# Performance work log

Hardware: AMD Instinct MI355X
Metric: run time of the kernel (lower is better)

## Reference

```python
import jax, jax.numpy as jnp
import numpy as np

B, N, H, E, P = 2, 20000, 128, 200000, 3


def _mlp2(x, w1, b1, w2, b2):
    # Linear -> SiLU -> Linear
    return jax.nn.silu(x @ w1 + b1) @ w2 + b2


def setup_inputs() -> dict:
    key = jax.random.key(0)
    ks = iter(jax.random.split(key, 40))
    def nrm(shape, s=0.05):
        return jax.random.normal(next(ks), shape, dtype=jnp.float32) * s
    inp = {
        "features": jax.random.normal(next(ks), (B, N, H), dtype=jnp.float32),
        "positions": jax.random.normal(next(ks), (B, N, P), dtype=jnp.float32),
        "edge_index_up": jax.random.randint(next(ks), (2, E), 0, N, dtype=jnp.int32),
        "edge_index_down": jax.random.randint(next(ks), (2, E), 0, N, dtype=jnp.int32),
        "degree_up": jax.random.uniform(next(ks), (N,), minval=1.0, maxval=32.0, dtype=jnp.float32),
        "degree_down": jax.random.uniform(next(ks), (N,), minval=1.0, maxval=32.0, dtype=jnp.float32),
    }
    for name in ("up", "down"):
        inp[f"w_msg1_{name}"] = nrm((2 * H + 1, H)); inp[f"b_msg1_{name}"] = jnp.zeros((H,), jnp.float32)
        inp[f"w_msg2_{name}"] = nrm((H, H));         inp[f"b_msg2_{name}"] = jnp.zeros((H,), jnp.float32)
        inp[f"w_pos1_{name}"] = nrm((H, H));         inp[f"b_pos1_{name}"] = jnp.zeros((H,), jnp.float32)
        inp[f"w_pos2_{name}"] = nrm((H, 1));         inp[f"b_pos2_{name}"] = jnp.zeros((1,), jnp.float32)
    inp["w_upd1"] = nrm((2 * H, H)); inp["b_upd1"] = jnp.zeros((H,), jnp.float32)
    inp["w_upd2"] = nrm((H, H));     inp["b_upd2"] = jnp.zeros((H,), jnp.float32)
    return inp


def reference(features, positions, edge_index_up, edge_index_down, degree_up, degree_down,
              w_msg1_up, b_msg1_up, w_msg2_up, b_msg2_up,
              w_pos1_up, b_pos1_up, w_pos2_up, b_pos2_up,
              w_msg1_down, b_msg1_down, w_msg2_down, b_msg2_down,
              w_pos1_down, b_pos1_down, w_pos2_down, b_pos2_down,
              w_upd1, b_upd1, w_upd2, b_upd2):
    n_neighborhoods = 2
    msg_acc = jnp.zeros_like(features)
    pos_upd = jnp.zeros_like(positions)
    neighborhoods = [
        (edge_index_up, degree_up,
         (w_msg1_up, b_msg1_up, w_msg2_up, b_msg2_up),
         (w_pos1_up, b_pos1_up, w_pos2_up, b_pos2_up)),
        (edge_index_down, degree_down,
         (w_msg1_down, b_msg1_down, w_msg2_down, b_msg2_down),
         (w_pos1_down, b_pos1_down, w_pos2_down, b_pos2_down)),
    ]
    for edge_index, degree, msg_p, pos_p in neighborhoods:
        src, dst = edge_index[0], edge_index[1]
        h_src = features[:, src, :]                     # [B, E, H] gather
        h_dst = features[:, dst, :]                     # [B, E, H] gather
        rel_pos = positions[:, src, :] - positions[:, dst, :]  # [B, E, P]
        dist = jnp.linalg.norm(rel_pos, axis=-1, keepdims=True)  # [B, E, 1]
        msg_input = jnp.concatenate([h_src, h_dst, dist], axis=-1)  # [B, E, 2H+1]
        messages = _mlp2(msg_input, *msg_p)             # [B, E, H]
        agg = jnp.zeros_like(features).at[:, dst, :].add(messages)  # scatter-add over dim 1
        agg = agg / jnp.clip(degree, 1.0, None)[None, :, None]
        msg_acc = msg_acc + agg
        weights = jnp.tanh(_mlp2(messages, *pos_p))     # [B, E, 1]
        pos_upd = pos_upd + jnp.zeros_like(positions).at[:, dst, :].add(weights * rel_pos)
    feat_update = _mlp2(jnp.concatenate([features, msg_acc], axis=-1), w_upd1, b_upd1, w_upd2, b_upd2)
    updated_features = features + feat_update
    updated_positions = positions + pos_upd / n_neighborhoods
    return updated_features, updated_positions
```

## Files before the change

kernel.cpp:

```cpp
#include <hip/hip_runtime.h>

#define BB 2
#define NN 20000
#define HH 128
#define EE 200000
#define EBLK 3125
#define NBLK 79

typedef unsigned short u16;
typedef __attribute__((ext_vector_type(4))) float f32x4;
typedef __bf16 bf16x8 __attribute__((ext_vector_type(8)));

#define MFMA(a, b, c) __builtin_amdgcn_mfma_f32_16x16x32_bf16((a), (b), (c), 0, 0, 0)

__device__ __forceinline__ float bf2f(u16 u) {
    union { unsigned int i; float f; } v; v.i = ((unsigned int)u) << 16; return v.f;
}
__device__ __forceinline__ u16 f2bf(float f) {
    union { __bf16 h; u16 u; } v; v.h = (__bf16)f; return v.u;
}
#if __has_builtin(__builtin_amdgcn_rcpf)
__device__ __forceinline__ float rcpf(float x) { return __builtin_amdgcn_rcpf(x); }
#else
__device__ __forceinline__ float rcpf(float x) { return 1.f / x; }
#endif
__device__ __forceinline__ float silu_f(float z) { return z * rcpf(1.f + __expf(-z)); }
__device__ __forceinline__ float ldv(const void* p, long i, int f) {
    return f ? ((const float*)p)[i] : bf2f(((const u16*)p)[i]);
}

__global__ __launch_bounds__(256) void detect_zero_kernel(const u16* __restrict__ f,
                                                          int* __restrict__ flag,
                                                          int* __restrict__ cnt) {
    int i = blockIdx.x * 256 + threadIdx.x;
    if (i < 40000) cnt[i] = 0;
    if (blockIdx.x == 0) {
        int tid = threadIdx.x;
        u16 v = f[tid * 2];
        int e = (v >> 7) & 0xFF;
        int ok = (e >= 101 && e <= 143) ? 1 : 0;
        __shared__ int c;
        if (tid == 0) c = 0;
        __syncthreads();
        atomicAdd(&c, ok);
        __syncthreads();
        if (tid == 0) *flag = (c < 200) ? 1 : 0;
    }
}

#define C5TOT 5281540
#define FTOT 180224
#define R0 5240000
#define R1 (R0 + C5TOT)
#define R2 (R1 + FTOT)
#define R3 (R2 + 2 * EE)
struct P18 { const void* p[18]; };
struct P8 { const void* w[8]; };

__global__ __launch_bounds__(256) void setup_kernel(
    P18 cp, P8 wf, const int* __restrict__ eu, const int* __restrict__ ed,
    float* __restrict__ ws_acc, u16* __restrict__ canon, u16* __restrict__ fbase,
    int* __restrict__ cnt_up, int* __restrict__ cnt_dn, const int* __restrict__ flag)
{
    long i = (long)blockIdx.x * 256 + threadIdx.x;
    if (i < R0) { ws_acc[i] = 0.f; return; }
    if (i < R1) {
        static const int off[19] = {
            0, 5120000, 5240000, 5260000, 5280000,
            5280128, 5280256, 5280384, 5280512, 5280640,
            5280642, 5280770, 5280898, 5281026, 5281154, 5281282,
            5281284, 5281412, 5281540 };
        static const int rsz[18] = {
            5120000, 120000, 20000, 20000,
            128, 128, 128, 128, 128, 1,
            128, 128, 128, 128, 128, 1,
            128, 128 };
        static const int soff[18] = {
            0, 0, 0, 0,
            32768, 0, 0, 0, 0, 0,
            32768, 0, 0, 0, 0, 0,
            0, 0 };
        int j = (int)(i - R0);
        int isf = *flag;
        int t = 0;
#pragma unroll 1
        while (j >= off[t + 1]) ++t;
        int k = j - off[t];
        u16 v = 0;
        if (k < rsz[t]) v = f2bf(ldv(cp.p[t], (long)soff[t] + k, isf));
        canon[j] = v;
        return;
    }
    if (i < R2) {
        static const int foff[9] = { 0, 32768, 49152, 65536, 98304, 114688,
                                     131072, 163840, 180224 };
        int j = (int)(i - R1);
        int isf = *flag;
        int t = 0;
#pragma unroll 1
        while (j >= foff[t + 1]) ++t;
        int m = j - foff[t];
        int jj = m & 7, lane = (m >> 3) & 63, nt = (m >> 9) & 7, kt = m >> 12;
        int k = kt * 32 + ((lane >> 4) * 8) + jj;
        int n = nt * 16 + (lane & 15);
        fbase[j] = f2bf(ldv(wf.w[t], (long)k * 128 + n, isf));
        return;
    }
    if (i < R3) {
        int e = (int)(i - R2);
        if (e < EE) atomicAdd(&cnt_up[eu[EE + e]], 1);
        else atomicAdd(&cnt_dn[ed[EE + e - EE]], 1);
    }
}

struct SP { const int* cnt[2]; int* cur[2]; int* bsum[2]; };

__global__ __launch_bounds__(256) void scan1_kernel(SP p) {
    int half = blockIdx.x / NBLK;
    int b = blockIdx.x - half * NBLK;
    int t = threadIdx.x;
    int i = b * 256 + t;
    __shared__ int buf[256];
    int v = (i < NN) ? p.cnt[half][i] : 0;
    buf[t] = v;
    __syncthreads();
    for (int s = 1; s < 256; s <<= 1) {
        int x = (t >= s) ? buf[t - s] : 0;
        __syncthreads();
        buf[t] += x;
        __syncthreads();
    }
    if (i < NN) p.cur[half][i] = buf[t] - v;
    if (t == 255) p.bsum[half][b] = buf[255];
}

__global__ __launch_bounds__(256) void scan2_kernel(int* __restrict__ bu, int* __restrict__ bd) {
    __shared__ int buf[2][128];
    int half = threadIdx.x >> 7, t = threadIdx.x & 127;
    int* bs = half ? bd : bu;
    int v = (t < NBLK) ? bs[t] : 0;
    buf[half][t] = v;
    __syncthreads();
    for (int s = 1; s < 128; s <<= 1) {
        int x = (t >= s) ? buf[half][t - s] : 0;
        __syncthreads();
        buf[half][t] += x;
        __syncthreads();
    }
    if (t < NBLK) bs[t] = buf[half][t] - v;
}

__global__ void scatter2_kernel(const int* __restrict__ eu, const int* __restrict__ ed,
                                int* __restrict__ cu, const int* __restrict__ bu,
                                int* __restrict__ cd, const int* __restrict__ bd,
                                int* __restrict__ su, int* __restrict__ sd) {
    int e = blockIdx.x * 256 + threadIdx.x;
    if (e < EE) {
        int d = eu[EE + e];
        int p = atomicAdd(&cu[d], 1) + bu[d >> 8];
        su[p] = e;
    } else {
        e -= EE;
        if (e < EE) {
            int d = ed[EE + e];
            int p = atomicAdd(&cd[d], 1) + bd[d >> 8];
            sd[p] = e;
        }
    }
}

struct EP {
    const int* eidx; const int* es; const u16* deg;
    const u16* fW1; const u16* fW2; const u16* fP1;
    const u16* w1last; const u16* bias1; const u16* bias2;
    const u16* biasp1; const u16* wp2; const u16* biasp2;
};

__global__ __launch_bounds__(512, 8) void edge_kernel(
    const u16* __restrict__ feat, const u16* __restrict__ posit,
    EP up, EP dn,
    float* __restrict__ msg_base, float* __restrict__ pos_base)
{
    const int tid = threadIdx.x;
    const int lane = tid & 63;
    const int wv = tid >> 6;
    const int half = blockIdx.x / (BB * EBLK);
    const int rem = blockIdx.x - half * (BB * EBLK);
    const int bb = rem / EBLK;
    const int s0 = (rem - bb * EBLK) * 64;
    const EP P = half ? dn : up;
    float* msg_acc = msg_base + (size_t)bb * NN * HH;
    float* pos_acc = pos_base + (size_t)bb * NN * 3;

    __shared__ u16 sX[64][136];
    __shared__ u16 sY[64][136];
    __shared__ float sRel[64][3];
    __shared__ float sDist[64];
    __shared__ float sInv[64];
    __shared__ int sDst[64];

    if (tid < 64) {
        int e = P.es[s0 + tid];
        int s = P.eidx[e];
        int d = P.eidx[EE + e];
        sDst[tid] = d;
        sInv[tid] = 1.f / fmaxf(bf2f(P.deg[d]), 1.f);
        const u16* ps = posit + ((size_t)bb * NN + s) * 3;
        const u16* pd = posit + ((size_t)bb * NN + d) * 3;
        float dx = bf2f(ps[0]) - bf2f(pd[0]);
        float dy = bf2f(ps[1]) - bf2f(pd[1]);
        float dz = bf2f(ps[2]) - bf2f(pd[2]);
        sRel[tid][0] = dx; sRel[tid][1] = dy; sRel[tid][2] = dz;
        sDist[tid] = sqrtf(dx * dx + dy * dy + dz * dz);
    }

    {
        const int r = tid >> 3, part = tid & 7;
        int e = P.es[s0 + r];
        int s = P.eidx[e];
        int d = P.eidx[EE + e];
        const uint4* fs = (const uint4*)(feat + ((size_t)bb * NN + s) * HH);
        const uint4* fd = (const uint4*)(feat + ((size_t)bb * NN + d) * HH);
        uint4* as = (uint4*)&sX[r][part * 16];
        uint4* ad = (uint4*)&sY[r][part * 16];
#pragma unroll
        for (int i = 0; i < 2; ++i) { as[i] = fs[part * 2 + i]; ad[i] = fd[part * 2 + i]; }
    }
    __syncthreads();

    const int nt = wv;
    const int mrow = lane & 15;
    const int kq = (lane >> 4) * 8;
    const int crow = (lane >> 4) * 4;
    const int ccol = lane & 15;
    const int col = nt * 16 + ccol;

    f32x4 acc[4];
#pragma unroll
    for (int mt = 0; mt < 4; ++mt) acc[mt] = (f32x4){0.f, 0.f, 0.f, 0.f};

#pragma unroll
    for (int kt = 0; kt < 8; ++kt) {
        const u16* Xb = (kt < 4) ? &sX[0][0] : &sY[0][0];
        const int kk = (kt & 3) * 32 + kq;
        bf16x8 bw = *(const bf16x8*)(P.fW1 + (size_t)(((kt * 8 + nt) * 64 + lane) * 8));
#pragma unroll
        for (int mt = 0; mt < 4; ++mt) {
            bf16x8 a = *(const bf16x8*)(Xb + (mt * 16 + mrow) * 136 + kk);
            acc[mt] = MFMA(a, bw, acc[mt]);
        }
    }
    __syncthreads();

    {
        const float wl = bf2f(P.w1last[col]);
        const float bb2 = bf2f(P.bias1[col]);
#pragma unroll
        for (int mt = 0; mt < 4; ++mt) {
#pragma unroll
            for (int r = 0; r < 4; ++r) {
                const int row = mt * 16 + crow + r;
                float z = fmaf(sDist[row], wl, acc[mt][r]) + bb2;
                sX[row][col] = f2bf(silu_f(z));
            }
        }
    }
    __syncthreads();

#pragma unroll
    for (int mt = 0; mt < 4; ++mt) acc[mt] = (f32x4){0.f, 0.f, 0.f, 0.f};
#pragma unroll
    for (int kt = 0; kt < 4; ++kt) {
        const int kk = kt * 32 + kq;
        bf16x8 bw = *(const bf16x8*)(P.fW2 + (size_t)(((kt * 8 + nt) * 64 + lane) * 8));
#pragma unroll
        for (int mt = 0; mt < 4; ++mt) {
            bf16x8 a = *(const bf16x8*)(&sX[0][0] + (mt * 16 + mrow) * 136 + kk);
            acc[mt] = MFMA(a, bw, acc[mt]);
        }
    }
    {
        const float bb2 = bf2f(P.bias2[col]);
#pragma unroll
        for (int mt = 0; mt < 4; ++mt) {
#pragma unroll
            for (int r = 0; r < 4; ++r) {
                const int row = mt * 16 + crow + r;
                sY[row][col] = f2bf(acc[mt][r] + bb2);
            }
        }
    }
    __syncthreads();

#pragma unroll
    for (int mt = 0; mt < 4; ++mt) acc[mt] = (f32x4){0.f, 0.f, 0.f, 0.f};
#pragma unroll
    for (int kt = 0; kt < 4; ++kt) {
        const int kk = kt * 32 + kq;
        bf16x8 bw = *(const bf16x8*)(P.fP1 + (size_t)(((kt * 8 + nt) * 64 + lane) * 8));
#pragma unroll
        for (int mt = 0; mt < 4; ++mt) {
            bf16x8 a = *(const bf16x8*)(&sY[0][0] + (mt * 16 + mrow) * 136 + kk);
            acc[mt] = MFMA(a, bw, acc[mt]);
        }
    }

    {
        const int scol = tid & 127;
        const int r0 = (tid >> 7) * 16;
        float accv = 0.f;
        int dprev = sDst[r0];
        float invprev = sInv[r0];
#pragma unroll 1
        for (int r = r0; r < r0 + 16; ++r) {
            int dcur = sDst[r];
            if (dcur != dprev) {
                unsafeAtomicAdd(&msg_acc[(size_t)dprev * HH + scol], accv * invprev);
                accv = 0.f; dprev = dcur; invprev = sInv[r];
            }
            accv += bf2f(sY[r][scol]);
        }
        unsafeAtomicAdd(&msg_acc[(size_t)dprev * HH + scol], accv * invprev);
    }

    {
        const float bb2 = bf2f(P.biasp1[col]);
#pragma unroll
        for (int mt = 0; mt < 4; ++mt) {
#pragma unroll
            for (int r = 0; r < 4; ++r) {
                const int row = mt * 16 + crow + r;
                sX[row][col] = f2bf(silu_f(acc[mt][r] + bb2));
            }
        }
    }
    __syncthreads();

    {
        const int r = tid >> 3, q = tid & 7;
        const unsigned* t32 = (const unsigned*)&sX[r][q * 16];
        const unsigned* w32 = (const unsigned*)(P.wp2 + q * 16);
        float p = 0.f;
#pragma unroll
        for (int k = 0; k < 8; ++k) {
            unsigned a = t32[k], b = w32[k];
            union { unsigned i; float f; } al, ah, bl, bh;
            al.i = a << 16; ah.i = a & 0xffff0000u;
            bl.i = b << 16; bh.i = b & 0xffff0000u;
            p = fmaf(al.f, bl.f, p);
            p = fmaf(ah.f, bh.f, p);
        }
        p += __shfl_xor(p, 1);
        p += __shfl_xor(p, 2);
        p += __shfl_xor(p, 4);
        if (q == 0) {
            float wgt = tanhf(p + bf2f(P.biasp2[0]));
            const size_t pb = (size_t)sDst[r] * 3;
            unsafeAtomicAdd(&pos_acc[pb + 0], wgt * sRel[r][0]);
            unsafeAtomicAdd(&pos_acc[pb + 1], wgt * sRel[r][1]);
            unsafeAtomicAdd(&pos_acc[pb + 2], wgt * sRel[r][2]);
        }
    }
}

__global__ __launch_bounds__(256) void update_kernel(
    const void* __restrict__ rawfeat, const void* __restrict__ rawpos,
    const u16* __restrict__ fU1, const u16* __restrict__ bu1,
    const u16* __restrict__ fU2, const u16* __restrict__ bu2,
    void* __restrict__ outp, const float* __restrict__ magg, const float* __restrict__ pacc,
    const int* __restrict__ flag)
{
    const int tid = threadIdx.x;
    const int lane = tid & 63;
    const int wv = tid >> 6;
    const int row0 = blockIdx.x * 64;
    const int isf = *flag;

    __shared__ u16 sA[64][136];
    __shared__ u16 sB[64][136];

    if (isf) {
        const float* fp = (const float*)rawfeat + (size_t)row0 * HH;
        for (int i = tid; i < 1024; i += 256) {
            int r = i >> 4, c = (i & 15) * 8;
            float4 v0 = *(const float4*)(fp + (size_t)r * HH + c);
            float4 v1 = *(const float4*)(fp + (size_t)r * HH + c + 4);
            uint4 o;
            o.x = (unsigned)f2bf(v0.x) | ((unsigned)f2bf(v0.y) << 16);
            o.y = (unsigned)f2bf(v0.z) | ((unsigned)f2bf(v0.w) << 16);
            o.z = (unsigned)f2bf(v1.x) | ((unsigned)f2bf(v1.y) << 16);
            o.w = (unsigned)f2bf(v1.z) | ((unsigned)f2bf(v1.w) << 16);
            *(uint4*)&sA[r][c] = o;
        }
    } else {
        const uint4* fp = (const uint4*)((const u16*)rawfeat + (size_t)row0 * HH);
        for (int i = tid; i < 1024; i += 256) {
            int r = i >> 4, c = i & 15;
            *(uint4*)&sA[r][c * 8] = fp[i];
        }
    }
    {
        const float4* am = (const float4*)(magg) + (size_t)row0 * 32;
        for (int i = tid; i < 2048; i += 256) {
            int r = i >> 5;
            float4 v = am[i];
            int c = (i & 31) * 4;
            sB[r][c + 0] = f2bf(v.x);
            sB[r][c + 1] = f2bf(v.y);
            sB[r][c + 2] = f2bf(v.z);
            sB[r][c + 3] = f2bf(v.w);
        }
    }
    __syncthreads();

    const int nt0 = wv * 2;
    const int mrow = lane & 15;
    const int kq = (lane >> 4) * 8;
    const int crow = (lane >> 4) * 4;
    const int ccol = lane & 15;

    f32x4 acc[4][2];
#pragma unroll
    for (int mt = 0; mt < 4; ++mt) {
        acc[mt][0] = (f32x4){0.f, 0.f, 0.f, 0.f};
        acc[mt][1] = (f32x4){0.f, 0.f, 0.f, 0.f};
    }
#pragma unroll
    for (int kt = 0; kt < 8; ++kt) {
        const u16* Xb = (kt < 4) ? &sA[0][0] : &sB[0][0];
        const int kk = (kt & 3) * 32 + kq;
        bf16x8 bw0 = *(const bf16x8*)(fU1 + (size_t)(((kt * 8 + nt0) * 64 + lane) * 8));
        bf16x8 bw1 = *(const bf16x8*)(fU1 + (size_t)(((kt * 8 + nt0 + 1) * 64 + lane) * 8));
#pragma unroll
        for (int mt = 0; mt < 4; ++mt) {
            bf16x8 a = *(const bf16x8*)(Xb + (mt * 16 + mrow) * 136 + kk);
            acc[mt][0] = MFMA(a, bw0, acc[mt][0]);
            acc[mt][1] = MFMA(a, bw1, acc[mt][1]);
        }
    }
    __syncthreads();

#pragma unroll
    for (int mt = 0; mt < 4; ++mt) {
#pragma unroll
        for (int n2 = 0; n2 < 2; ++n2) {
            const int col = (nt0 + n2) * 16 + ccol;
            const float bb = bf2f(bu1[col]);
#pragma unroll
            for (int r = 0; r < 4; ++r) {
                const int row = mt * 16 + crow + r;
                sB[row][col] = f2bf(silu_f(acc[mt][n2][r] + bb));
            }
        }
    }
    __syncthreads();

#pragma unroll
    for (int mt = 0; mt < 4; ++mt) {
        acc[mt][0] = (f32x4){0.f, 0.f, 0.f, 0.f};
        acc[mt][1] = (f32x4){0.f, 0.f, 0.f, 0.f};
    }
#pragma unroll
    for (int kt = 0; kt < 4; ++kt) {
        const int kk = kt * 32 + kq;
        bf16x8 bw0 = *(const bf16x8*)(fU2 + (size_t)(((kt * 8 + nt0) * 64 + lane) * 8));
        bf16x8 bw1 = *(const bf16x8*)(fU2 + (size_t)(((kt * 8 + nt0 + 1) * 64 + lane) * 8));
#pragma unroll
        for (int mt = 0; mt < 4; ++mt) {
            bf16x8 a = *(const bf16x8*)(&sB[0][0] + (mt * 16 + mrow) * 136 + kk);
            acc[mt][0] = MFMA(a, bw0, acc[mt][0]);
            acc[mt][1] = MFMA(a, bw1, acc[mt][1]);
        }
    }
#pragma unroll
    for (int mt = 0; mt < 4; ++mt) {
#pragma unroll
        for (int n2 = 0; n2 < 2; ++n2) {
            const int col = (nt0 + n2) * 16 + ccol;
            const float bb = bf2f(bu2[col]);
#pragma unroll
            for (int r = 0; r < 4; ++r) {
                const int row = mt * 16 + crow + r;
                const size_t idx = (size_t)(row0 + row) * HH + col;
                if (isf) {
                    float base = ((const float*)rawfeat)[idx];
                    ((float*)outp)[idx] = acc[mt][n2][r] + bb + base;
                } else {
                    float base = bf2f(sA[row][col]);
                    ((u16*)outp)[idx] = f2bf(acc[mt][n2][r] + bb + base);
                }
            }
        }
    }

    if (tid < 192) {
        int i = row0 * 3 + tid;
        float x = pacc[i];
        if (isf) {
            float base = ((const float*)rawpos)[i];
            ((float*)outp)[5120000 + i] = base + 0.5f * x;
        } else {
            float base = bf2f(((const u16*)rawpos)[i]);
            ((u16*)outp)[5120000 + i] = f2bf(base + 0.5f * x);
        }
    }
}

extern "C" void kernel_launch(void* const* d_in, const int* in_sizes, int n_in,
                              void* d_out, int out_size, void* d_ws, size_t ws_size,
                              hipStream_t stream)
{
    float* ws_msg  = (float*)d_ws;
    float* ws_pos  = (float*)((char*)d_ws + 20480000);
    int*   cnt_up  = (int*)((char*)d_ws + 20960000);
    int*   cnt_dn  = (int*)((char*)d_ws + 21040000);
    int*   cur_up  = (int*)((char*)d_ws + 21120000);
    int*   cur_dn  = (int*)((char*)d_ws + 21200000);
    int*   bsum_up = (int*)((char*)d_ws + 21280000);
    int*   bsum_dn = (int*)((char*)d_ws + 21280400);
    int*   es_up   = (int*)((char*)d_ws + 21280800);
    int*   es_dn   = (int*)((char*)d_ws + 22080800);
    u16*   fbase   = (u16*)((char*)d_ws + 22880800);
    u16*   canon   = (u16*)((char*)d_ws + 23241248);
    int*   flag    = (int*)((char*)d_ws + 33804328);
    if (ws_size < 33804332ULL) return;

    u16* f_m1u = fbase;
    u16* f_m2u = fbase + 32768;
    u16* f_p1u = fbase + 49152;
    u16* f_m1d = fbase + 65536;
    u16* f_m2d = fbase + 98304;
    u16* f_p1d = fbase + 114688;
    u16* f_u1  = fbase + 131072;
    u16* f_u2  = fbase + 163840;

    u16* cfeat  = canon;
    u16* cpos   = canon + 5120000;
    u16* cdgu   = canon + 5240000;
    u16* cdgd   = canon + 5260000;
    u16* cw1lu  = canon + 5280000;
    u16* cb1u   = canon + 5280128;
    u16* cb2u   = canon + 5280256;
    u16* cbp1u  = canon + 5280384;
    u16* cwp2u  = canon + 5280512;
    u16* cbp2u  = canon + 5280640;
    u16* cw1ld  = canon + 5280642;
    u16* cb1d   = canon + 5280770;
    u16* cb2d   = canon + 5280898;
    u16* cbp1d  = canon + 5281026;
    u16* cwp2d  = canon + 5281154;
    u16* cbp2d  = canon + 5281282;
    u16* cbu1   = canon + 5281284;
    u16* cbu2   = canon + 5281412;

    const int* ei_up = (const int*)d_in[2];
    const int* ei_dn = (const int*)d_in[3];

    detect_zero_kernel<<<157, 256, 0, stream>>>((const u16*)d_in[0], flag, cnt_up);

    P18 cp;
    cp.p[0] = d_in[0];  cp.p[1] = d_in[1];  cp.p[2] = d_in[4];  cp.p[3] = d_in[5];
    cp.p[4] = d_in[6];  cp.p[5] = d_in[7];  cp.p[6] = d_in[9];  cp.p[7] = d_in[11];
    cp.p[8] = d_in[12]; cp.p[9] = d_in[13];
    cp.p[10] = d_in[14]; cp.p[11] = d_in[15]; cp.p[12] = d_in[17]; cp.p[13] = d_in[19];
    cp.p[14] = d_in[20]; cp.p[15] = d_in[21];
    cp.p[16] = d_in[23]; cp.p[17] = d_in[25];
    P8 wsf;
    wsf.w[0] = d_in[6];  wsf.w[1] = d_in[8];  wsf.w[2] = d_in[10]; wsf.w[3] = d_in[14];
    wsf.w[4] = d_in[16]; wsf.w[5] = d_in[18]; wsf.w[6] = d_in[22]; wsf.w[7] = d_in[24];
    setup_kernel<<<(R3 + 255) / 256, 256, 0, stream>>>(cp, wsf, ei_up, ei_dn,
                                                       ws_msg, canon, fbase,
                                                       cnt_up, cnt_dn, flag);

    SP sp;
    sp.cnt[0] = cnt_up; sp.cnt[1] = cnt_dn;
    sp.cur[0] = cur_up; sp.cur[1] = cur_dn;
    sp.bsum[0] = bsum_up; sp.bsum[1] = bsum_dn;
    scan1_kernel<<<2 * NBLK, 256, 0, stream>>>(sp);
    scan2_kernel<<<1, 256, 0, stream>>>(bsum_up, bsum_dn);
    scatter2_kernel<<<(2 * EE + 255) / 256, 256, 0, stream>>>(ei_up, ei_dn, cur_up, bsum_up,
                                                              cur_dn, bsum_dn, es_up, es_dn);

    EP up, dn;
    up.eidx = ei_up; up.es = es_up; up.deg = cdgu;
    up.fW1 = f_m1u; up.fW2 = f_m2u; up.fP1 = f_p1u;
    up.w1last = cw1lu; up.bias1 = cb1u; up.bias2 = cb2u;
    up.biasp1 = cbp1u; up.wp2 = cwp2u; up.biasp2 = cbp2u;
    dn.eidx = ei_dn; dn.es = es_dn; dn.deg = cdgd;
    dn.fW1 = f_m1d; dn.fW2 = f_m2d; dn.fP1 = f_p1d;
    dn.w1last = cw1ld; dn.bias1 = cb1d; dn.bias2 = cb2d;
    dn.biasp1 = cbp1d; dn.wp2 = cwp2d; dn.biasp2 = cbp2d;
    edge_kernel<<<2 * BB * EBLK, 512, 0, stream>>>(cfeat, cpos, up, dn, ws_msg, ws_pos);

    update_kernel<<<625, 256, 0, stream>>>(d_in[0], d_in[1], f_u1, cbu1, f_u2, cbu2,
                                           d_out, ws_msg, ws_pos, flag);
}
```

Measured before the change: 517.3 us.

## Make edge kernel persistent over 8 tiles with double-buffered gather prefetch

Each block now processes eight 64-edge tiles in sequence instead of one. The feature and position gathers for the next tile are issued into registers before the first MFMA stage and stored into the alternate shared-memory buffer afterwards. The aim is to hide the random gather latency behind the MLP compute and to cut block launch overhead. In exchange, shared memory per block doubles, launch bounds drop to 4 blocks, and fewer blocks are resident, so there is less parallelism across blocks. The last block pads out of range tiles with inactive iterations.

```diff
diff --git a/kernel.cpp b/kernel.cpp
--- a/kernel.cpp
+++ b/kernel.cpp
@@ -5,6 +5,9 @@
 #define HH 128
 #define EE 200000
 #define EBLK 3125
+#define TILES 12500
+#define TPB 8
+#define EGRID 1563
 #define NBLK 79
 
 typedef unsigned short u16;
@@ -176,7 +179,7 @@
     const u16* biasp1; const u16* wp2; const u16* biasp2;
 };
 
-__global__ __launch_bounds__(512, 8) void edge_kernel(
+__global__ __launch_bounds__(512, 4) void edge_kernel(
     const u16* __restrict__ feat, const u16* __restrict__ posit,
     EP up, EP dn,
     float* __restrict__ msg_base, float* __restrict__ pos_base)
@@ -184,49 +187,14 @@
     const int tid = threadIdx.x;
     const int lane = tid & 63;
     const int wv = tid >> 6;
-    const int half = blockIdx.x / (BB * EBLK);
-    const int rem = blockIdx.x - half * (BB * EBLK);
-    const int bb = rem / EBLK;
-    const int s0 = (rem - bb * EBLK) * 64;
-    const EP P = half ? dn : up;
-    float* msg_acc = msg_base + (size_t)bb * NN * HH;
-    float* pos_acc = pos_base + (size_t)bb * NN * 3;
-
-    __shared__ u16 sX[64][136];
-    __shared__ u16 sY[64][136];
-    __shared__ float sRel[64][3];
-    __shared__ float sDist[64];
-    __shared__ float sInv[64];
-    __shared__ int sDst[64];
-
-    if (tid < 64) {
-        int e = P.es[s0 + tid];
-        int s = P.eidx[e];
-        int d = P.eidx[EE + e];
-        sDst[tid] = d;
-        sInv[tid] = 1.f / fmaxf(bf2f(P.deg[d]), 1.f);
-        const u16* ps = posit + ((size_t)bb * NN + s) * 3;
-        const u16* pd = posit + ((size_t)bb * NN + d) * 3;
-        float dx = bf2f(ps[0]) - bf2f(pd[0]);
-        float dy = bf2f(ps[1]) - bf2f(pd[1]);
-        float dz = bf2f(ps[2]) - bf2f(pd[2]);
-        sRel[tid][0] = dx; sRel[tid][1] = dy; sRel[tid][2] = dz;
-        sDist[tid] = sqrtf(dx * dx + dy * dy + dz * dz);
-    }
-
-    {
-        const int r = tid >> 3, part = tid & 7;
-        int e = P.es[s0 + r];
-        int s = P.eidx[e];
-        int d = P.eidx[EE + e];
-        const uint4* fs = (const uint4*)(feat + ((size_t)bb * NN + s) * HH);
-        const uint4* fd = (const uint4*)(feat + ((size_t)bb * NN + d) * HH);
-        uint4* as = (uint4*)&sX[r][part * 16];
-        uint4* ad = (uint4*)&sY[r][part * 16];
-#pragma unroll
-        for (int i = 0; i < 2; ++i) { as[i] = fs[part * 2 + i]; ad[i] = fd[part * 2 + i]; }
-    }
-    __syncthreads();
+    const int tile0 = blockIdx.x * TPB;
+
+    __shared__ u16 sX[2][64][136];
+    __shared__ u16 sY[2][64][136];
+    __shared__ float sRel[2][64][3];
+    __shared__ float sDist[2][64];
+    __shared__ float sInv[2][64];
+    __shared__ int sDst[2][64];
 
     const int nt = wv;
     const int mrow = lane & 15;
@@ -234,131 +202,232 @@
     const int crow = (lane >> 4) * 4;
     const int ccol = lane & 15;
     const int col = nt * 16 + ccol;
-
-    f32x4 acc[4];
-#pragma unroll
-    for (int mt = 0; mt < 4; ++mt) acc[mt] = (f32x4){0.f, 0.f, 0.f, 0.f};
-
-#pragma unroll
-    for (int kt = 0; kt < 8; ++kt) {
-        const u16* Xb = (kt < 4) ? &sX[0][0] : &sY[0][0];
-        const int kk = (kt & 3) * 32 + kq;
-        bf16x8 bw = *(const bf16x8*)(P.fW1 + (size_t)(((kt * 8 + nt) * 64 + lane) * 8));
-#pragma unroll
-        for (int mt = 0; mt < 4; ++mt) {
-            bf16x8 a = *(const bf16x8*)(Xb + (mt * 16 + mrow) * 136 + kk);
-            acc[mt] = MFMA(a, bw, acc[mt]);
-        }
-    }
-    __syncthreads();
+    const int gr = tid >> 3, gpart = tid & 7;
 
     {
-        const float wl = bf2f(P.w1last[col]);
-        const float bb2 = bf2f(P.bias1[col]);
-#pragma unroll
-        for (int mt = 0; mt < 4; ++mt) {
-#pragma unroll
-            for (int r = 0; r < 4; ++r) {
-                const int row = mt * 16 + crow + r;
-                float z = fmaf(sDist[row], wl, acc[mt][r]) + bb2;
-                sX[row][col] = f2bf(silu_f(z));
-            }
-        }
-    }
-    __syncthreads();
-
-#pragma unroll
-    for (int mt = 0; mt < 4; ++mt) acc[mt] = (f32x4){0.f, 0.f, 0.f, 0.f};
-#pragma unroll
-    for (int kt = 0; kt < 4; ++kt) {
-        const int kk = kt * 32 + kq;
-        bf16x8 bw = *(const bf16x8*)(P.fW2 + (size_t)(((kt * 8 + nt) * 64 + lane) * 8));
-#pragma unroll
-        for (int mt = 0; mt < 4; ++mt) {
-            bf16x8 a = *(const bf16x8*)(&sX[0][0] + (mt * 16 + mrow) * 136 + kk);
-            acc[mt] = MFMA(a, bw, acc[mt]);
-        }
-    }
-    {
-        const float bb2 = bf2f(P.bias2[col]);
-#pragma unroll
-        for (int mt = 0; mt < 4; ++mt) {
-#pragma unroll
-            for (int r = 0; r < 4; ++r) {
-                const int row = mt * 16 + crow + r;
-                sY[row][col] = f2bf(acc[mt][r] + bb2);
-            }
-        }
-    }
-    __syncthreads();
-
-#pragma unroll
-    for (int mt = 0; mt < 4; ++mt) acc[mt] = (f32x4){0.f, 0.f, 0.f, 0.f};
-#pragma unroll
-    for (int kt = 0; kt < 4; ++kt) {
-        const int kk = kt * 32 + kq;
-        bf16x8 bw = *(const bf16x8*)(P.fP1 + (size_t)(((kt * 8 + nt) * 64 + lane) * 8));
-#pragma unroll
-        for (int mt = 0; mt < 4; ++mt) {
-            bf16x8 a = *(const bf16x8*)(&sY[0][0] + (mt * 16 + mrow) * 136 + kk);
-            acc[mt] = MFMA(a, bw, acc[mt]);
-        }
-    }
-
-    {
-        const int scol = tid & 127;
-        const int r0 = (tid >> 7) * 16;
-        float accv = 0.f;
-        int dprev = sDst[r0];
-        float invprev = sInv[r0];
+        int tile = tile0;
+        int half = tile / (2 * EBLK);
+        int rem = tile - half * (2 * EBLK);
+        int bb = rem / EBLK;
+        int s0 = (rem - bb * EBLK) * 64;
+        const EP Q = half ? dn : up;
+        {
+            int e = Q.es[s0 + gr];
+            int s = Q.eidx[e];
+            int d = Q.eidx[EE + e];
+            const uint4* fs = (const uint4*)(feat + ((size_t)bb * NN + s) * HH);
+            const uint4* fd = (const uint4*)(feat + ((size_t)bb * NN + d) * HH);
+            *(uint4*)&sX[0][gr][gpart * 16] = fs[gpart * 2];
+            *(uint4*)&sX[0][gr][gpart * 16 + 8] = fs[gpart * 2 + 1];
+            *(uint4*)&sY[0][gr][gpart * 16] = fd[gpart * 2];
+            *(uint4*)&sY[0][gr][gpart * 16 + 8] = fd[gpart * 2 + 1];
+        }
+        if (tid < 64) {
+            int e = Q.es[s0 + tid];
+            int s = Q.eidx[e];
+            int d = Q.eidx[EE + e];
+            sDst[0][tid] = d;
+            sInv[0][tid] = 1.f / fmaxf(bf2f(Q.deg[d]), 1.f);
+            const u16* ps = posit + ((size_t)bb * NN + s) * 3;
+            const u16* pd = posit + ((size_t)bb * NN + d) * 3;
+            float dx = bf2f(ps[0]) - bf2f(pd[0]);
+            float dy = bf2f(ps[1]) - bf2f(pd[1]);
+            float dz = bf2f(ps[2]) - bf2f(pd[2]);
+            sRel[0][tid][0] = dx; sRel[0][tid][1] = dy; sRel[0][tid][2] = dz;
+            sDist[0][tid] = sqrtf(dx * dx + dy * dy + dz * dz);
+        }
+    }
+
 #pragma unroll 1
-        for (int r = r0; r < r0 + 16; ++r) {
-            int dcur = sDst[r];
-            if (dcur != dprev) {
-                unsafeAtomicAdd(&msg_acc[(size_t)dprev * HH + scol], accv * invprev);
-                accv = 0.f; dprev = dcur; invprev = sInv[r];
-            }
-            accv += bf2f(sY[r][scol]);
-        }
-        unsafeAtomicAdd(&msg_acc[(size_t)dprev * HH + scol], accv * invprev);
-    }
-
-    {
-        const float bb2 = bf2f(P.biasp1[col]);
-#pragma unroll
-        for (int mt = 0; mt < 4; ++mt) {
-#pragma unroll
-            for (int r = 0; r < 4; ++r) {
-                const int row = mt * 16 + crow + r;
-                sX[row][col] = f2bf(silu_f(acc[mt][r] + bb2));
-            }
-        }
-    }
-    __syncthreads();
-
-    {
-        const int r = tid >> 3, q = tid & 7;
-        const unsigned* t32 = (const unsigned*)&sX[r][q * 16];
-        const unsigned* w32 = (const unsigned*)(P.wp2 + q * 16);
-        float p = 0.f;
-#pragma unroll
-        for (int k = 0; k < 8; ++k) {
-            unsigned a = t32[k], b = w32[k];
-            union { unsigned i; float f; } al, ah, bl, bh;
-            al.i = a << 16; ah.i = a & 0xffff0000u;
-            bl.i = b << 16; bh.i = b & 0xffff0000u;
-            p = fmaf(al.f, bl.f, p);
-            p = fmaf(ah.f, bh.f, p);
-        }
-        p += __shfl_xor(p, 1);
-        p += __shfl_xor(p, 2);
-        p += __shfl_xor(p, 4);
-        if (q == 0) {
-            float wgt = tanhf(p + bf2f(P.biasp2[0]));
-            const size_t pb = (size_t)sDst[r] * 3;
-            unsafeAtomicAdd(&pos_acc[pb + 0], wgt * sRel[r][0]);
-            unsafeAtomicAdd(&pos_acc[pb + 1], wgt * sRel[r][1]);
-            unsafeAtomicAdd(&pos_acc[pb + 2], wgt * sRel[r][2]);
+    for (int t = 0; t < TPB; ++t) {
+        int tile = tile0 + t;
+        const bool active = (tile < TILES);
+        if (!active) tile = TILES - 1;
+        int half = tile / (2 * EBLK);
+        int rem = tile - half * (2 * EBLK);
+        int bb = rem / EBLK;
+        const EP P = half ? dn : up;
+        float* msg_acc = msg_base + (size_t)bb * NN * HH;
+        float* pos_acc = pos_base + (size_t)bb * NN * 3;
+        const int p = t & 1;
+
+        __syncthreads();
+
+        const bool dopre = (t < TPB - 1);
+        uint4 g0, g1, g2, g3;
+        float m_rx = 0.f, m_ry = 0.f, m_rz = 0.f, m_dist = 0.f, m_inv = 0.f;
+        int m_dst = 0;
+        if (dopre) {
+            int ntile = tile0 + t + 1;
+            if (ntile >= TILES) ntile = TILES - 1;
+            int nhalf = ntile / (2 * EBLK);
+            int nrem = ntile - nhalf * (2 * EBLK);
+            int nbb = nrem / EBLK;
+            int ns0 = (nrem - nbb * EBLK) * 64;
+            const EP Q = nhalf ? dn : up;
+            {
+                int e = Q.es[ns0 + gr];
+                int s = Q.eidx[e];
+                int d = Q.eidx[EE + e];
+                const uint4* fs = (const uint4*)(feat + ((size_t)nbb * NN + s) * HH);
+                const uint4* fd = (const uint4*)(feat + ((size_t)nbb * NN + d) * HH);
+                g0 = fs[gpart * 2]; g1 = fs[gpart * 2 + 1];
+                g2 = fd[gpart * 2]; g3 = fd[gpart * 2 + 1];
+            }
+            if (tid < 64) {
+                int e = Q.es[ns0 + tid];
+                int s = Q.eidx[e];
+                int d = Q.eidx[EE + e];
+                m_dst = d;
+                m_inv = 1.f / fmaxf(bf2f(Q.deg[d]), 1.f);
+                const u16* ps = posit + ((size_t)nbb * NN + s) * 3;
+                const u16* pd = posit + ((size_t)nbb * NN + d) * 3;
+                m_rx = bf2f(ps[0]) - bf2f(pd[0]);
+                m_ry = bf2f(ps[1]) - bf2f(pd[1]);
+                m_rz = bf2f(ps[2]) - bf2f(pd[2]);
+                m_dist = sqrtf(m_rx * m_rx + m_ry * m_ry + m_rz * m_rz);
+            }
+        }
+
+        f32x4 acc[4];
+#pragma unroll
+        for (int mt = 0; mt < 4; ++mt) acc[mt] = (f32x4){0.f, 0.f, 0.f, 0.f};
+
+#pragma unroll
+        for (int kt = 0; kt < 8; ++kt) {
+            const u16* Xb = (kt < 4) ? &sX[p][0][0] : &sY[p][0][0];
+            const int kk = (kt & 3) * 32 + kq;
+            bf16x8 bw = *(const bf16x8*)(P.fW1 + (size_t)(((kt * 8 + nt) * 64 + lane) * 8));
+#pragma unroll
+            for (int mt = 0; mt < 4; ++mt) {
+                bf16x8 a = *(const bf16x8*)(Xb + (mt * 16 + mrow) * 136 + kk);
+                acc[mt] = MFMA(a, bw, acc[mt]);
+            }
+        }
+        __syncthreads();
+
+        if (dopre) {
+            const int q2 = p ^ 1;
+            *(uint4*)&sX[q2][gr][gpart * 16] = g0;
+            *(uint4*)&sX[q2][gr][gpart * 16 + 8] = g1;
+            *(uint4*)&sY[q2][gr][gpart * 16] = g2;
+            *(uint4*)&sY[q2][gr][gpart * 16 + 8] = g3;
+            if (tid < 64) {
+                sDst[q2][tid] = m_dst;
+                sInv[q2][tid] = m_inv;
+                sRel[q2][tid][0] = m_rx; sRel[q2][tid][1] = m_ry; sRel[q2][tid][2] = m_rz;
+                sDist[q2][tid] = m_dist;
+            }
+        }
+
+        {
+            const float wl = bf2f(P.w1last[col]);
+            const float bb2 = bf2f(P.bias1[col]);
+#pragma unroll
+            for (int mt = 0; mt < 4; ++mt) {
+#pragma unroll
+                for (int r = 0; r < 4; ++r) {
+                    const int row = mt * 16 + crow + r;
+                    float z = fmaf(sDist[p][row], wl, acc[mt][r]) + bb2;
+                    sX[p][row][col] = f2bf(silu_f(z));
+                }
+            }
+        }
+        __syncthreads();
+
+#pragma unroll
+        for (int mt = 0; mt < 4; ++mt) acc[mt] = (f32x4){0.f, 0.f, 0.f, 0.f};
+#pragma unroll
+        for (int kt = 0; kt < 4; ++kt) {
+            const int kk = kt * 32 + kq;
+            bf16x8 bw = *(const bf16x8*)(P.fW2 + (size_t)(((kt * 8 + nt) * 64 + lane) * 8));
+#pragma unroll
+            for (int mt = 0; mt < 4; ++mt) {
+                bf16x8 a = *(const bf16x8*)(&sX[p][0][0] + (mt * 16 + mrow) * 136 + kk);
+                acc[mt] = MFMA(a, bw, acc[mt]);
+            }
+        }
+        {
+            const float bb2 = bf2f(P.bias2[col]);
+#pragma unroll
+            for (int mt = 0; mt < 4; ++mt) {
+#pragma unroll
+                for (int r = 0; r < 4; ++r) {
+                    const int row = mt * 16 + crow + r;
+                    sY[p][row][col] = f2bf(acc[mt][r] + bb2);
+                }
+            }
+        }
+        __syncthreads();
+
+#pragma unroll
+        for (int mt = 0; mt < 4; ++mt) acc[mt] = (f32x4){0.f, 0.f, 0.f, 0.f};
+#pragma unroll
+        for (int kt = 0; kt < 4; ++kt) {
+            const int kk = kt * 32 + kq;
+            bf16x8 bw = *(const bf16x8*)(P.fP1 + (size_t)(((kt * 8 + nt) * 64 + lane) * 8));
+#pragma unroll
+            for (int mt = 0; mt < 4; ++mt) {
+                bf16x8 a = *(const bf16x8*)(&sY[p][0][0] + (mt * 16 + mrow) * 136 + kk);
+                acc[mt] = MFMA(a, bw, acc[mt]);
+            }
+        }
+
+        if (active) {
+            const int scol = tid & 127;
+            const int r0 = (tid >> 7) * 16;
+            float accv = 0.f;
+            int dprev = sDst[p][r0];
+            float invprev = sInv[p][r0];
+#pragma unroll 1
+            for (int r = r0; r < r0 + 16; ++r) {
+                int dcur = sDst[p][r];
+                if (dcur != dprev) {
+                    unsafeAtomicAdd(&msg_acc[(size_t)dprev * HH + scol], accv * invprev);
+                    accv = 0.f; dprev = dcur; invprev = sInv[p][r];
+                }
+                accv += bf2f(sY[p][r][scol]);
+            }
+            unsafeAtomicAdd(&msg_acc[(size_t)dprev * HH + scol], accv * invprev);
+        }
+
+        {
+            const float bb2 = bf2f(P.biasp1[col]);
+#pragma unroll
+            for (int mt = 0; mt < 4; ++mt) {
+#pragma unroll
+                for (int r = 0; r < 4; ++r) {
+                    const int row = mt * 16 + crow + r;
+                    sX[p][row][col] = f2bf(silu_f(acc[mt][r] + bb2));
+                }
+            }
+        }
+        __syncthreads();
+
+        {
+            const int r = tid >> 3, q = tid & 7;
+            const unsigned* t32 = (const unsigned*)&sX[p][r][q * 16];
+            const unsigned* w32 = (const unsigned*)(P.wp2 + q * 16);
+            float pp = 0.f;
+#pragma unroll
+            for (int k = 0; k < 8; ++k) {
+                unsigned a = t32[k], b = w32[k];
+                union { unsigned i; float f; } al, ah, bl, bh;
+                al.i = a << 16; ah.i = a & 0xffff0000u;
+                bl.i = b << 16; bh.i = b & 0xffff0000u;
+                pp = fmaf(al.f, bl.f, pp);
+                pp = fmaf(ah.f, bh.f, pp);
+            }
+            pp += __shfl_xor(pp, 1);
+            pp += __shfl_xor(pp, 2);
+            pp += __shfl_xor(pp, 4);
+            if (q == 0 && active) {
+                float wgt = tanhf(pp + bf2f(P.biasp2[0]));
+                const size_t pb = (size_t)sDst[p][r] * 3;
+                unsafeAtomicAdd(&pos_acc[pb + 0], wgt * sRel[p][r][0]);
+                unsafeAtomicAdd(&pos_acc[pb + 1], wgt * sRel[p][r][1]);
+                unsafeAtomicAdd(&pos_acc[pb + 2], wgt * sRel[p][r][2]);
+            }
         }
     }
 }
@@ -590,7 +659,7 @@
     dn.fW1 = f_m1d; dn.fW2 = f_m2d; dn.fP1 = f_p1d;
     dn.w1last = cw1ld; dn.bias1 = cb1d; dn.bias2 = cb2d;
     dn.biasp1 = cbp1d; dn.wp2 = cwp2d; dn.biasp2 = cbp2d;
-    edge_kernel<<<2 * BB * EBLK, 512, 0, stream>>>(cfeat, cpos, up, dn, ws_msg, ws_pos);
+    edge_kernel<<<EGRID, 512, 0, stream>>>(cfeat, cpos, up, dn, ws_msg, ws_pos);
 
     update_kernel<<<625, 256, 0, stream>>>(d_in[0], d_in[1], f_u1, cbu1, f_u2, cbu2,
                                            d_out, ws_msg, ws_pos, flag);
```

Measured after the change: 620.5 us. 19.9% more time.
